# Optimization experiments

Measured on AMD Instinct MI355X. Metric: run time of the kernel, lower is better.

Reference implementation:

```python
import jax, jax.numpy as jnp
import numpy as np

_DN = ('NCHW', 'OIHW', 'NCHW')

def _conv(x, w, b, stride, pad):
    y = jax.lax.conv_general_dilated(x, w, (stride, stride), [(pad, pad), (pad, pad)], dimension_numbers=_DN)
    return y + b[None, :, None, None]

def setup_inputs() -> dict:
    key = jax.random.key(0)
    ks = jax.random.split(key, 9)
    B, C, H, W = 32, 3, 128, 128
    HC, D, K = 128, 64, 512
    def he(k, shape, fan_in):
        return jax.random.normal(k, shape, jnp.float32) * np.float32(np.sqrt(2.0 / fan_in))
    return {
        'x': jax.random.normal(ks[0], (B, C, H, W), jnp.float32),
        'enc_w1': he(ks[1], (HC, C, 3, 3), C * 9),
        'enc_b1': jnp.zeros((HC,), jnp.float32),
        'enc_w2': he(ks[2], (HC, HC, 3, 3), HC * 9),
        'enc_b2': jnp.zeros((HC,), jnp.float32),
        'proj_w': he(ks[3], (D, HC, 1, 1), HC),
        'proj_b': jnp.zeros((D,), jnp.float32),
        'codebook': jax.random.uniform(ks[4], (K, D), jnp.float32, -1.0 / K, 1.0 / K),
        'dproj_w': he(ks[5], (HC, D, 1, 1), D),
        'dproj_b': jnp.zeros((HC,), jnp.float32),
        'dconv1_w': he(ks[6], (HC, HC, 3, 3), HC * 9),
        'dconv1_b': jnp.zeros((HC,), jnp.float32),
        'dconv2_w': he(ks[7], (C, HC, 1, 1), HC),
        'dconv2_b': jnp.zeros((C,), jnp.float32),
    }

def reference(x, enc_w1, enc_b1, enc_w2, enc_b2, proj_w, proj_b, codebook,
              dproj_w, dproj_b, dconv1_w, dconv1_b, dconv2_w, dconv2_b):
    beta = 0.25
    Gh = Gw = 8
    B, C, H, W = x.shape
    D = codebook.shape[1]
    sg = jax.lax.stop_gradient
    # ---- encoder ----
    h = jax.nn.relu(_conv(x, enc_w1, enc_b1, 2, 1))      # (B,HC,H/2,W/2)
    h = jax.nn.relu(_conv(h, enc_w2, enc_b2, 2, 1))      # (B,HC,H/4,W/4)
    f = h.shape[2] // Gh                                  # adaptive avg pool (exact)
    h = h.reshape(B, h.shape[1], Gh, f, Gw, f).mean(axis=(3, 5))
    z_e = _conv(h, proj_w, proj_b, 1, 0)                 # (B,D,Gh,Gw)
    # ---- vector quantizer ----
    z_flat = z_e.transpose(0, 2, 3, 1).reshape(-1, D)    # (B*Gh*Gw, D)
    dist = ((z_flat ** 2).sum(1, keepdims=True)
            + (codebook ** 2).sum(1)[None, :]
            - 2.0 * (z_flat @ codebook.T))               # (N, K)
    idx_flat = jnp.argmin(dist, axis=1)
    z_q_flat = codebook[idx_flat]                        # gather
    codebook_loss = jnp.mean((z_q_flat - sg(z_flat)) ** 2)
    commit_loss = jnp.mean((z_flat - sg(z_q_flat)) ** 2)
    vq_loss = codebook_loss + beta * commit_loss
    z_q_st = z_flat + sg(z_q_flat - z_flat)              # straight-through
    z_q = z_q_st.reshape(B, Gh, Gw, D).transpose(0, 3, 1, 2)
    idx = idx_flat.reshape(B, Gh, Gw)
    # ---- decoder ----
    y = _conv(z_q, dproj_w, dproj_b, 1, 0)               # (B,HC,Gh,Gw)
    s = H // Gh                                           # nearest upsample factor
    y = jnp.repeat(jnp.repeat(y, s, axis=2), s, axis=3)  # (B,HC,H,W)
    y = jax.nn.relu(y)
    y = jax.nn.relu(_conv(y, dconv1_w, dconv1_b, 1, 1))
    x_hat = _conv(y, dconv2_w, dconv2_b, 1, 0)           # (B,C,H,W)
    return (x_hat, idx, vq_loss, z_e)
```

## Files before the change

### kernel.cpp

```cpp
#include <hip/hip_runtime.h>
#include <math.h>


typedef _Float16 f16x8 __attribute__((ext_vector_type(8)));
typedef float f32x4 __attribute__((ext_vector_type(4)));

#define H1N 16777216
#define YTAIL (2048 * 128)

__global__ __launch_bounds__(256) void k_prep(const float* __restrict__ w2,
                                              const float* __restrict__ w1,
                                              const float* __restrict__ wp,
                                              const float* __restrict__ wd,
                                              const float* __restrict__ wd1,
                                              const float* __restrict__ cb,
                                              float* __restrict__ w1t,
                                              float* __restrict__ wpT,
                                              float* __restrict__ wdT,
                                              float* __restrict__ cbT,
                                              _Float16* __restrict__ Ah,
                                              _Float16* __restrict__ WS,
                                              _Float16* __restrict__ h1h) {
  int bx = blockIdx.x, tid = threadIdx.x;
  if (bx < 128) {
    __shared__ float wrow[1152];
    int co = bx;
    for (int i = tid; i < 1152; i += 256) wrow[i] = wd1[co * 1152 + i];
    __syncthreads();
    if (tid < 128) {
      int ci = tid;
      float w[9];
#pragma unroll
      for (int t = 0; t < 9; t++) w[t] = wrow[ci * 9 + t];
      float rx[3][5];
#pragma unroll
      for (int ky = 0; ky < 3; ky++) {
        float a0 = w[ky * 3 + 0], a1 = w[ky * 3 + 1], a2 = w[ky * 3 + 2];
        rx[ky][0] = a0; rx[ky][1] = a1 + a2; rx[ky][2] = a0 + a1 + a2;
        rx[ky][3] = a0 + a1; rx[ky][4] = a2;
      }
#pragma unroll
      for (int px = 0; px < 5; px++) {
        float s0 = rx[0][px], s1 = rx[1][px], s2 = rx[2][px];
        float ry[5];
        ry[0] = s0; ry[1] = s1 + s2; ry[2] = s0 + s1 + s2; ry[3] = s0 + s1; ry[4] = s2;
#pragma unroll
        for (int py = 0; py < 5; py++) {
          int pq = py * 5 + px;
          int o = (pq * 128 + co) * 128 + ci;
          Ah[o] = (_Float16)ry[py];
        }
      }
    }
    return;
  }
  if (bx < 144) {
    __shared__ float wst[9216];
    int co0 = (bx - 128) * 8;
    for (int i = tid; i < 9216; i += 256) wst[i] = w2[co0 * 1152 + i];
    __syncthreads();
    for (int i = tid; i < 9216; i += 256) {
      int co = i / 1152, r = i - co * 1152;
      int tap = r >> 7, ci = r & 127;
      float v = wst[co * 1152 + ci * 9 + tap];
      int og = ((tap * 16 + (ci >> 3)) * 128 + co0 + co) * 8 + (ci & 7);
      WS[og] = (_Float16)v;
    }
    return;
  }
  if (bx < 152) {
    __shared__ float cbs[64 * 65];
    int k0 = (bx - 144) * 64;
    for (int i = tid; i < 4096; i += 256) {
      int k = i >> 6, d = i & 63;
      cbs[k * 65 + d] = cb[(k0 + k) * 64 + d];
    }
    __syncthreads();
    for (int i = tid; i < 4096; i += 256) {
      int d = i >> 6, k = i & 63;
      cbT[d * 512 + k0 + k] = cbs[k * 65 + d];
    }
    return;
  }
  for (int i = tid; i < 3456; i += 256) {
    int co = i & 127, t = i >> 7;
    w1t[t * 128 + co] = w1[co * 27 + t];
  }
  for (int i = tid; i < 8192; i += 256) {
    int d = i & 63, k = i >> 6;
    wpT[k * 64 + d] = wp[d * 128 + k];
  }
  for (int i = tid; i < 8192; i += 256) {
    int co = i & 127, d = i >> 7;
    wdT[d * 128 + co] = wd[co * 64 + d];
  }
  if (tid < 64) h1h[H1N + tid] = (_Float16)0.f;
}

__global__ __launch_bounds__(256) void k_conv1(const float* __restrict__ x,
                                               const float* __restrict__ w1t,
                                               const float* __restrict__ b1,
                                               _Float16* __restrict__ h1h) {
  __shared__ float E[3][9][68];
  __shared__ float O[3][9][68];
  int co_t = blockIdx.x, oh_t = blockIdx.y, b = blockIdx.z;
  int oh0 = oh_t * 4;
  int tid = threadIdx.x;
  int wv = __builtin_amdgcn_readfirstlane(tid >> 6);
  int l = tid & 63;
  int coB = co_t * 32 + wv * 8;

  for (int idx = tid; idx < 1728; idx += 256) {
    int p = idx & 63, r = idx >> 6;
    int ci = r / 9, lr = r - ci * 9;
    int ih = 2 * oh0 - 1 + lr;
    float2 v = make_float2(0.f, 0.f);
    if ((unsigned)ih < 128u)
      v = *(const float2*)&x[((b * 3 + ci) * 128 + ih) * 128 + 2 * p];
    E[ci][lr][p] = v.x;
    O[ci][lr][p + 1] = v.y;
  }
  if (tid < 27) {
    int ci = tid / 9, lr = tid - ci * 9;
    O[ci][lr][0] = 0.f;
  }
  __syncthreads();

  int ohl = l >> 4, ow0 = (l & 15) * 4;
  int oh = oh0 + ohl;
  float4 acc[8];
#pragma unroll
  for (int q = 0; q < 8; q++) {
    float bv = b1[coB + q];
    acc[q] = make_float4(bv, bv, bv, bv);
  }
#pragma unroll
  for (int ci = 0; ci < 3; ci++) {
#pragma unroll
    for (int ky = 0; ky < 3; ky++) {
      int lr = 2 * ohl + ky;
      float4 ev = *(float4*)&E[ci][lr][ow0];
      float4 od = *(float4*)&O[ci][lr][ow0];
      float o4 = O[ci][lr][ow0 + 4];
      const float* wr = w1t + (ci * 9 + ky * 3) * 128 + coB;
#pragma unroll
      for (int q = 0; q < 8; q++) {
        float wa = wr[q], wb = wr[128 + q], wc = wr[256 + q];
        acc[q].x = fmaf(wa, od.x, acc[q].x);
        acc[q].x = fmaf(wb, ev.x, acc[q].x);
        acc[q].x = fmaf(wc, od.y, acc[q].x);
        acc[q].y = fmaf(wa, od.y, acc[q].y);
        acc[q].y = fmaf(wb, ev.y, acc[q].y);
        acc[q].y = fmaf(wc, od.z, acc[q].y);
        acc[q].z = fmaf(wa, od.z, acc[q].z);
        acc[q].z = fmaf(wb, ev.z, acc[q].z);
        acc[q].z = fmaf(wc, od.w, acc[q].z);
        acc[q].w = fmaf(wa, od.w, acc[q].w);
        acc[q].w = fmaf(wb, ev.w, acc[q].w);
        acc[q].w = fmaf(wc, o4,   acc[q].w);
      }
    }
  }
  int g = coB >> 3;
  int pbase = ((g * 32 + b) * 64 + oh) * 64;
#pragma unroll
  for (int oi = 0; oi < 4; oi++) {
    f16x8 hv;
#pragma unroll
    for (int q = 0; q < 8; q++)
      hv[q] = (_Float16)fmaxf(((const float*)&acc[q])[oi], 0.f);
    *(f16x8*)&h1h[(pbase + ow0 + oi) * 8] = hv;
  }
}

#define C2_ACHUNK 4420
#define C2_WCHUNK 2340
#define C2_WOFF (C2_ACHUNK * 8)
#define C2_LDSB ((C2_ACHUNK + C2_WCHUNK) * 16)
#define C2_STEP 4194304
#define C2_WADV 4096

__global__ __launch_bounds__(512, 2) void k_conv2(const _Float16* __restrict__ h1h,
                                                  const _Float16* __restrict__ WS,
                                                  const float* __restrict__ b2,
                                                  float* __restrict__ h2p) {
  extern __shared__ _Float16 L[];
  int bx = blockIdx.x;
  int cohalf = bx & 1;
  int bq = bx >> 1;
  int b = bq >> 2, ohq = bq & 3;
  int oh0 = ohq * 8;
  int tid = threadIdx.x;
  int w = tid >> 6, l = tid & 63;
  int cw = w & 1, rw = w >> 1;
  int ln = l & 15, quad = l >> 4;

  int cursA[9];
  int advA[9];
#pragma unroll
  for (int k = 0; k < 9; k++) {
    int c = (k < 8) ? (tid + k * 512) : (4096 + tid);
    if (c < C2_ACHUNK) {
      int q = c / 65, rem = c - q * 65;
      int ph = rem >= 33;
      int u = ph ? rem - 33 : rem;
      int r = q % 17, g = q / 17;
      int iw = ph ? 2 * u : 2 * u - 1;
      int ih = 2 * oh0 - 1 + r;
      bool ok = (ih >= 0) && (iw >= 0) && (iw < 64);
      cursA[k] = ok ? ((g * 32 + b) * 64 + ih) * 512 + iw * 8 : H1N;
      advA[k] = ok ? C2_STEP : 0;
    } else {
      cursA[k] = H1N;
      advA[k] = 0;
    }
  }
  int cursW[5];
#pragma unroll
  for (int k = 0; k < 5; k++) {
    int c = (k < 4) ? (tid + k * 512) : (2048 + tid);
    if (c < C2_WCHUNK) {
      int q65 = c / 65, u = c - q65 * 65;
      if (u > 63) u = 63;
      int t = q65 >> 2, ci8 = q65 & 3;
      cursW[k] = (t * 16 + ci8) * 1024 + (cohalf * 64 + u) * 8;
    } else {
      cursW[k] = 0;
    }
  }

  f32x4 acc[2][4] = {};
  for (int step = 0; step < 4; step++) {
    if (step) __syncthreads();
#pragma unroll
    for (int k = 0; k < 8; k++) {
      __builtin_amdgcn_global_load_lds(
          (const __attribute__((address_space(1))) void*)(h1h + cursA[k]),
          (__attribute__((address_space(3))) void*)&L[(tid + k * 512) * 8],
          16, 0, 0);
      cursA[k] += advA[k];
    }
    if (tid < 324)
      __builtin_amdgcn_global_load_lds(
          (const __attribute__((address_space(1))) void*)(h1h + cursA[8]),
          (__attribute__((address_space(3))) void*)&L[(4096 + tid) * 8],
          16, 0, 0);
    cursA[8] += advA[8];
#pragma unroll
    for (int k = 0; k < 4; k++) {
      __builtin_amdgcn_global_load_lds(
          (const __attribute__((address_space(1))) void*)(WS + cursW[k]),
          (__attribute__((address_space(3))) void*)&L[C2_WOFF +
                                                     (tid + k * 512) * 8],
          16, 0, 0);
      cursW[k] += C2_WADV;
    }
    if (tid < 292)
      __builtin_amdgcn_global_load_lds(
          (const __attribute__((address_space(1))) void*)(WS + cursW[4]),
          (__attribute__((address_space(3))) void*)&L[C2_WOFF +
                                                     (2048 + tid) * 8],
          16, 0, 0);
    cursW[4] += C2_WADV;
    __syncthreads();

#pragma unroll
    for (int ky = 0; ky < 3; ky++) {
#pragma unroll
      for (int kx = 0; kx < 3; kx++) {
        int t = ky * 3 + kx;
        int wb = (t * 4 + quad) * 65 + cw * 32 + ln;
        f16x8 Ah0 = *(const f16x8*)&L[C2_WOFF + wb * 8];
        f16x8 Ah1 = *(const f16x8*)&L[C2_WOFF + (wb + 16) * 8];
#pragma unroll
        for (int s = 0; s < 4; s++) {
          int owl = (s & 1) * 16 + ln;
          int r = 4 * rw + 2 * (s >> 1) + ky;
          int abase = (quad * 17 + r) * 65;
          int uoff = (kx == 1) ? (33 + owl) : (owl + (kx == 2));
          f16x8 Bh = *(const f16x8*)&L[(abase + uoff) * 8];
          acc[0][s] = __builtin_amdgcn_mfma_f32_16x16x32_f16(Ah0, Bh, acc[0][s], 0, 0, 0);
          acc[1][s] = __builtin_amdgcn_mfma_f32_16x16x32_f16(Ah1, Bh, acc[1][s], 0, 0, 0);
        }
      }
    }
  }
  __syncthreads();
  float* h2s = (float*)L;
#pragma unroll
  for (int cs = 0; cs < 2; cs++)
#pragma unroll
    for (int s = 0; s < 4; s++) {
      int row = 2 * rw + (s >> 1);
      int col = (s & 1) * 16 + ln;
#pragma unroll
      for (int r2 = 0; r2 < 4; r2++) {
        int co64 = cw * 32 + cs * 16 + quad * 4 + r2;
        int co = cohalf * 64 + co64;
        h2s[(co64 * 8 + row) * 32 + col] = fmaxf(acc[cs][s][r2] + b2[co], 0.f);
      }
    }
  __syncthreads();
  for (int c = tid; c < 1024; c += 512) {
    int co64 = c >> 4, rem = c & 15;
    int pr = rem >> 3, pc = rem & 7;
    const float* base = &h2s[(co64 * 8 + pr * 4) * 32 + pc * 4];
    float s = 0.f;
#pragma unroll
    for (int rr = 0; rr < 4; rr++) {
      s += base[rr * 32 + 0];
      s += base[rr * 32 + 1];
      s += base[rr * 32 + 2];
      s += base[rr * 32 + 3];
    }
    h2p[((b * 128 + cohalf * 64 + co64) * 8 + (2 * ohq + pr)) * 8 + pc] =
        s * 0.0625f;
  }
}

__global__ __launch_bounds__(256) void k_poolproj(const float* __restrict__ h2p,
                                                  const float* __restrict__ wpT,
                                                  const float* __restrict__ pb,
                                                  float* __restrict__ z_e_out,
                                                  float* __restrict__ lossacc) {
  __shared__ float hp[128][16];
  __shared__ float Ws[128][64];
  int bx = blockIdx.x, tid = threadIdx.x;
  int b = bx >> 2, quarter = bx & 3;
  if (bx == 0 && tid == 0) lossacc[0] = 0.f;
  for (int i = tid; i < 8192; i += 256) Ws[i >> 6][i & 63] = wpT[i];
  for (int i = tid; i < 2048; i += 256) {
    int ci = i >> 4, pl = i & 15;
    hp[ci][pl] = h2p[(b * 128 + ci) * 64 + quarter * 16 + pl];
  }
  __syncthreads();
  int d = tid >> 2, s0 = (tid & 3) * 4;
  float4 acc = make_float4(0.f, 0.f, 0.f, 0.f);
  for (int k = 0; k < 128; k++) {
    float a = Ws[k][d];
    float4 h = *(float4*)&hp[k][s0];
    acc.x = fmaf(a, h.x, acc.x);
    acc.y = fmaf(a, h.y, acc.y);
    acc.z = fmaf(a, h.z, acc.z);
    acc.w = fmaf(a, h.w, acc.w);
  }
  float bv = pb[d];
  float4 r4 = make_float4(acc.x + bv, acc.y + bv, acc.z + bv, acc.w + bv);
  *(float4*)&z_e_out[(b * 64 + d) * 64 + quarter * 16 + s0] = r4;
}

__global__ __launch_bounds__(256) void k_vqdproj(const float* __restrict__ z_e,
                                                 const float* __restrict__ cbT,
                                                 const float* __restrict__ cb,
                                                 const float* __restrict__ wdT,
                                                 const float* __restrict__ db,
                                                 float* __restrict__ idx_f,
                                                 _Float16* __restrict__ Yh,
                                                 float* __restrict__ loss_acc) {
  __shared__ float zs[64];
  __shared__ float zqv[64];
  __shared__ double wbst[4];
  __shared__ int wbi[4];
  int n = blockIdx.x, tid = threadIdx.x;
  int b = n >> 6, pi = n & 63;
  if (tid < 64) zs[tid] = z_e[(b * 64 + tid) * 64 + pi];
  if (n == 0 && tid < 64) {
    Yh[YTAIL + tid] = (_Float16)0.f;
    Yh[YTAIL + 64 + tid] = (_Float16)0.f;
  }
  __syncthreads();
  int w = tid >> 6, lane = tid & 63;
  double best = 1e300;
  int bi = 0;
#pragma unroll
  for (int j = 0; j < 2; j++) {
    int k = w * 128 + j * 64 + lane;
    double a0 = 0.0, a1 = 0.0, a2 = 0.0, a3 = 0.0;
#pragma unroll 4
    for (int d = 0; d < 64; d += 4) {
      double f0 = (double)zs[d] - (double)cbT[d * 512 + k];
      double f1 = (double)zs[d + 1] - (double)cbT[(d + 1) * 512 + k];
      double f2 = (double)zs[d + 2] - (double)cbT[(d + 2) * 512 + k];
      double f3 = (double)zs[d + 3] - (double)cbT[(d + 3) * 512 + k];
      a0 = fma(f0, f0, a0);
      a1 = fma(f1, f1, a1);
      a2 = fma(f2, f2, a2);
      a3 = fma(f3, f3, a3);
    }
    double acc = (a0 + a1) + (a2 + a3);
    if (acc < best) { best = acc; bi = k; }
  }
  for (int m = 1; m < 64; m <<= 1) {
    double ob = __shfl_xor(best, m, 64);
    int oi = __shfl_xor(bi, m, 64);
    if (ob < best || (ob == best && oi < bi)) { best = ob; bi = oi; }
  }
  if (lane == 0) { wbst[w] = best; wbi[w] = bi; }
  __syncthreads();
  best = wbst[0];
  bi = wbi[0];
#pragma unroll
  for (int q = 1; q < 4; q++) {
    double ob = wbst[q];
    int oi = wbi[q];
    if (ob < best || (ob == best && oi < bi)) { best = ob; bi = oi; }
  }
  if (tid < 64) {
    float zq_l = cb[bi * 64 + tid];
    float e = zq_l - zs[tid];
    float sq = e * e;
    for (int m = 1; m < 64; m <<= 1) sq += __shfl_xor(sq, m, 64);
    if (tid == 0) {
      idx_f[n] = (float)bi;
      atomicAdd(loss_acc, sq);
    }
    zqv[tid] = zq_l;
  }
  __syncthreads();
  if (tid < 128) {
    float a = db[tid];
#pragma unroll 4
    for (int d = 0; d < 64; d++) a = fmaf(wdT[d * 128 + tid], zqv[d], a);
    Yh[n * 128 + tid] = (_Float16)fmaxf(a, 0.f);
  }
}

__global__ __launch_bounds__(256) void k_dec(const _Float16* __restrict__ Yh,
                                             const _Float16* __restrict__ Ah,
                                             const float* __restrict__ bc1,
                                             float* __restrict__ Tb) {
  int bxx = blockIdx.x;
  int cls = bxx >> 6, n_t = bxx & 63;
  int rc = cls / 3, c3 = cls - rc * 3;
  const int rset[3][2] = {{0, 1}, {2, 2}, {3, 4}};
  const int rcnt[3] = {2, 1, 2};
  int w = threadIdx.x >> 6, l = threadIdx.x & 63;
  int ln = l & 15, quad = l >> 4;
  int coW = w * 32;
  int nB = n_t * 32;
  int kq = quad * 8;
  f32x4 acc[2][2] = {};
  for (int iy = 0; iy < rcnt[rc]; iy++) {
    int py = rset[rc][iy];
    int dy = (py == 0) ? -1 : ((py == 4) ? 1 : 0);
    for (int ix = 0; ix < rcnt[c3]; ix++) {
      int px = rset[c3][ix];
      int dx = (px == 0) ? -1 : ((px == 4) ? 1 : 0);
      int pq = py * 5 + px;
      int src[2];
#pragma unroll
      for (int s = 0; s < 2; s++) {
        int n = nB + s * 16 + ln;
        int bb = n >> 6, s6 = n & 63;
        int sy = (s6 >> 3) + dy, sx = (s6 & 7) + dx;
        bool ok = ((unsigned)sy < 8u) && ((unsigned)sx < 8u);
        src[s] = ok ? ((bb * 64 + sy * 8 + sx) * 128) : YTAIL;
      }
#pragma unroll 2
      for (int ci0 = 0; ci0 < 128; ci0 += 32) {
        const int wbase = (pq * 128 + coW + ln) * 128 + ci0 + kq;
        f16x8 Ah0 = *(const f16x8*)&Ah[wbase];
        f16x8 Ah1 = *(const f16x8*)&Ah[wbase + 2048];
        f16x8 Bh[2];
#pragma unroll
        for (int s = 0; s < 2; s++)
          Bh[s] = *(const f16x8*)&Yh[src[s] + ci0 + kq];
#pragma unroll
        for (int cs = 0; cs < 2; cs++) {
          f16x8 ah = cs ? Ah1 : Ah0;
#pragma unroll
          for (int s = 0; s < 2; s++)
            acc[cs][s] = __builtin_amdgcn_mfma_f32_16x16x32_f16(ah, Bh[s], acc[cs][s], 0, 0, 0);
        }
      }
    }
  }
#pragma unroll
  for (int cs = 0; cs < 2; cs++)
#pragma unroll
    for (int s = 0; s < 2; s++) {
      int site = nB + s * 16 + ln;
      int co0 = coW + cs * 16 + quad * 4;
      float4 bv = *(const float4*)&bc1[co0];
      float4 g = make_float4(fmaxf(acc[cs][s][0] + bv.x, 0.f),
                             fmaxf(acc[cs][s][1] + bv.y, 0.f),
                             fmaxf(acc[cs][s][2] + bv.z, 0.f),
                             fmaxf(acc[cs][s][3] + bv.w, 0.f));
      *(float4*)&Tb[(cls * 2048 + site) * 128 + co0] = g;
    }
}

__global__ __launch_bounds__(256) void k_out(const float* __restrict__ TbG,
                                             const float* __restrict__ w3,
                                             const float* __restrict__ b3,
                                             float* __restrict__ xhat,
                                             const float* __restrict__ loss_acc,
                                             float* __restrict__ out_loss) {
  __shared__ float Tb[9][128];
  __shared__ float part[9][3][8];
  __shared__ float vals[9][3];
  int bj = blockIdx.x, bi = blockIdx.y, b = blockIdx.z;
  int s = bi * 8 + bj;
  int n = b * 64 + s;
  int tid = threadIdx.x;
  if (bj == 0 && bi == 0 && b == 0 && tid == 0)
    out_loss[0] = loss_acc[0] * 1.25f / 131072.0f;
  for (int i = tid; i < 1152; i += 256) {
    int cls = i >> 7, co = i & 127;
    Tb[cls][co] = TbG[(cls * 2048 + n) * 128 + co];
  }
  __syncthreads();
  if (tid < 216) {
    int cls = tid / 24, rem = tid - cls * 24;
    int cc = rem >> 3, seg = rem & 7;
    float ss = 0.f;
#pragma unroll
    for (int d = 0; d < 16; d++) ss = fmaf(w3[cc * 128 + seg * 16 + d], Tb[cls][seg * 16 + d], ss);
    part[cls][cc][seg] = ss;
  }
  __syncthreads();
  if (tid < 27) {
    int cls = tid / 3, cc = tid - cls * 3;
    float ss = b3[cc];
#pragma unroll
    for (int seg = 0; seg < 8; seg++) ss += part[cls][cc][seg];
    vals[cls][cc] = ss;
  }
  __syncthreads();
  for (int i = tid; i < 768; i += 256) {
    int cc = i >> 8, p = i & 255;
    int ry = p >> 4, rx = p & 15;
    int rcls = (ry == 0) ? 0 : ((ry == 15) ? 2 : 1);
    int ccls = (rx == 0) ? 0 : ((rx == 15) ? 2 : 1);
    xhat[((b * 3 + cc) * 128 + bi * 16 + ry) * 128 + bj * 16 + rx] =
        vals[rcls * 3 + ccls][cc];
  }
}

extern "C" void kernel_launch(void* const* d_in, const int* in_sizes, int n_in,
                              void* d_out, int out_size, void* d_ws, size_t ws_size,
                              hipStream_t stream) {
  const float* x   = (const float*)d_in[0];
  const float* w1  = (const float*)d_in[1];
  const float* b1  = (const float*)d_in[2];
  const float* w2  = (const float*)d_in[3];
  const float* b2  = (const float*)d_in[4];
  const float* wp  = (const float*)d_in[5];
  const float* pb  = (const float*)d_in[6];
  const float* cb  = (const float*)d_in[7];
  const float* wd  = (const float*)d_in[8];
  const float* db  = (const float*)d_in[9];
  const float* wc1 = (const float*)d_in[10];
  const float* bc1 = (const float*)d_in[11];
  const float* wc2 = (const float*)d_in[12];
  const float* bc2 = (const float*)d_in[13];
  float* out = (float*)d_out;
  float* ws  = (float*)d_ws;

  _Float16* h1h = (_Float16*)(ws);
  float* h2p    = ws + 16777280;
  _Float16* WS  = (_Float16*)(ws + 20971584);
  float* w1t    = ws + 21119040;
  float* wpT    = ws + 21122496;
  float* wdT    = ws + 21130688;
  float* cbT    = ws + 21138880;
  _Float16* Ahd = (_Float16*)(ws + 21171648);
  float* Tb      = ws;
  _Float16* Yh   = (_Float16*)(ws + 6553600);
  float* lossacc = ws + 6815872;

  float* o_xhat = out;
  float* o_idx  = out + 1572864;
  float* o_loss = out + 1574912;
  float* o_ze   = out + 1574913;

  static bool s_attr_done = false;
  if (!s_attr_done) {
    (void)hipFuncSetAttribute((const void*)k_conv2,
                              hipFuncAttributeMaxDynamicSharedMemorySize, C2_LDSB);
    s_attr_done = true;
  }

  k_prep<<<dim3(153), 256, 0, stream>>>(w2, w1, wp, wd, wc1, cb,
                                        w1t, wpT, wdT, cbT, Ahd, WS, h1h);
  k_conv1<<<dim3(4, 16, 32), 256, 0, stream>>>(x, w1t, b1, h1h);
  k_conv2<<<dim3(256), 512, C2_LDSB, stream>>>(h1h, WS, b2, h2p);
  k_poolproj<<<dim3(128), 256, 0, stream>>>(h2p, wpT, pb, o_ze, lossacc);
  k_vqdproj<<<dim3(2048), 256, 0, stream>>>(o_ze, cbT, cb, wdT, db, o_idx, Yh, lossacc);
  k_dec<<<dim3(576), 256, 0, stream>>>(Yh, Ahd, bc1, Tb);
  k_out<<<dim3(8, 8, 32), 256, 0, stream>>>(Tb, wc2, bc2, o_xhat, lossacc, o_loss);
}
```

Before: 201.9 us.

## Rewrite first encoder conv as fp16 MFMA implicit GEMM

The first conv (3->128 channels, stride 2) moves from scalar fp32 FMAs to an im2col-in-LDS implicit GEMM using 16x16x32 f16 MFMA, with K=27 padded to 32. The weights are pre-packed as fp16 in the prep kernel, and each block now handles one output row for all 128 output channels. Outputs go through an LDS tile so the grouped fp16 layout is written with wide stores. This lowers the input and weights to fp16 precision before the multiply, which adds rounding error against the fp32 reference.

```diff
diff --git a/kernel.cpp b/kernel.cpp
--- a/kernel.cpp
+++ b/kernel.cpp
@@ -2,6 +2,7 @@
 #include <math.h>
 
 
+typedef _Float16 f16x4 __attribute__((ext_vector_type(4)));
 typedef _Float16 f16x8 __attribute__((ext_vector_type(8)));
 typedef float f32x4 __attribute__((ext_vector_type(4)));
 
@@ -14,7 +15,7 @@
                                               const float* __restrict__ wd,
                                               const float* __restrict__ wd1,
                                               const float* __restrict__ cb,
-                                              float* __restrict__ w1t,
+                                              _Float16* __restrict__ w1A,
                                               float* __restrict__ wpT,
                                               float* __restrict__ wdT,
                                               float* __restrict__ cbT,
@@ -82,9 +83,9 @@
     }
     return;
   }
-  for (int i = tid; i < 3456; i += 256) {
-    int co = i & 127, t = i >> 7;
-    w1t[t * 128 + co] = w1[co * 27 + t];
+  for (int i = tid; i < 4096; i += 256) {
+    int co = i >> 5, k = i & 31;
+    w1A[i] = (k < 27) ? (_Float16)w1[co * 27 + k] : (_Float16)0.f;
   }
   for (int i = tid; i < 8192; i += 256) {
     int d = i & 63, k = i >> 6;
@@ -98,78 +99,77 @@
 }
 
 __global__ __launch_bounds__(256) void k_conv1(const float* __restrict__ x,
-                                               const float* __restrict__ w1t,
+                                               const _Float16* __restrict__ w1A,
                                                const float* __restrict__ b1,
                                                _Float16* __restrict__ h1h) {
-  __shared__ float E[3][9][68];
-  __shared__ float O[3][9][68];
-  int co_t = blockIdx.x, oh_t = blockIdx.y, b = blockIdx.z;
-  int oh0 = oh_t * 4;
+  __shared__ _Float16 xs[3][3][132];
+  __shared__ _Float16 J[64 * 40];
+  __shared__ _Float16 As[128 * 40];
+  __shared__ _Float16 Cs[64 * 136];
+  int oh = blockIdx.x, b = blockIdx.y;
   int tid = threadIdx.x;
-  int wv = __builtin_amdgcn_readfirstlane(tid >> 6);
-  int l = tid & 63;
-  int coB = co_t * 32 + wv * 8;
-
-  for (int idx = tid; idx < 1728; idx += 256) {
-    int p = idx & 63, r = idx >> 6;
-    int ci = r / 9, lr = r - ci * 9;
-    int ih = 2 * oh0 - 1 + lr;
-    float2 v = make_float2(0.f, 0.f);
-    if ((unsigned)ih < 128u)
-      v = *(const float2*)&x[((b * 3 + ci) * 128 + ih) * 128 + 2 * p];
-    E[ci][lr][p] = v.x;
-    O[ci][lr][p + 1] = v.y;
-  }
-  if (tid < 27) {
-    int ci = tid / 9, lr = tid - ci * 9;
-    O[ci][lr][0] = 0.f;
-  }
-  __syncthreads();
-
-  int ohl = l >> 4, ow0 = (l & 15) * 4;
-  int oh = oh0 + ohl;
-  float4 acc[8];
-#pragma unroll
-  for (int q = 0; q < 8; q++) {
-    float bv = b1[coB + q];
-    acc[q] = make_float4(bv, bv, bv, bv);
-  }
-#pragma unroll
-  for (int ci = 0; ci < 3; ci++) {
-#pragma unroll
-    for (int ky = 0; ky < 3; ky++) {
-      int lr = 2 * ohl + ky;
-      float4 ev = *(float4*)&E[ci][lr][ow0];
-      float4 od = *(float4*)&O[ci][lr][ow0];
-      float o4 = O[ci][lr][ow0 + 4];
-      const float* wr = w1t + (ci * 9 + ky * 3) * 128 + coB;
-#pragma unroll
-      for (int q = 0; q < 8; q++) {
-        float wa = wr[q], wb = wr[128 + q], wc = wr[256 + q];
-        acc[q].x = fmaf(wa, od.x, acc[q].x);
-        acc[q].x = fmaf(wb, ev.x, acc[q].x);
-        acc[q].x = fmaf(wc, od.y, acc[q].x);
-        acc[q].y = fmaf(wa, od.y, acc[q].y);
-        acc[q].y = fmaf(wb, ev.y, acc[q].y);
-        acc[q].y = fmaf(wc, od.z, acc[q].y);
-        acc[q].z = fmaf(wa, od.z, acc[q].z);
-        acc[q].z = fmaf(wb, ev.z, acc[q].z);
-        acc[q].z = fmaf(wc, od.w, acc[q].z);
-        acc[q].w = fmaf(wa, od.w, acc[q].w);
-        acc[q].w = fmaf(wb, ev.w, acc[q].w);
-        acc[q].w = fmaf(wc, o4,   acc[q].w);
-      }
-    }
-  }
-  int g = coB >> 3;
-  int pbase = ((g * 32 + b) * 64 + oh) * 64;
-#pragma unroll
-  for (int oi = 0; oi < 4; oi++) {
-    f16x8 hv;
-#pragma unroll
-    for (int q = 0; q < 8; q++)
-      hv[q] = (_Float16)fmaxf(((const float*)&acc[q])[oi], 0.f);
-    *(f16x8*)&h1h[(pbase + ow0 + oi) * 8] = hv;
+  int w = tid >> 6, l = tid & 63;
+  int ln = l & 15, quad = l >> 4;
+  int coW = w * 32;
+  int kq = quad * 8;
+
+  for (int i = tid; i < 1152; i += 256) {
+    int ci = i / 384, rem = i - ci * 384;
+    int r = rem >> 7, iw = rem & 127;
+    int ih = 2 * oh - 1 + r;
+    float v = ((unsigned)ih < 128u) ? x[((b * 3 + ci) * 128 + ih) * 128 + iw] : 0.f;
+    xs[ci][r][1 + iw] = (_Float16)v;
+  }
+  if (tid < 9) {
+    int ci = tid / 3, r = tid - ci * 3;
+    xs[ci][r][0] = (_Float16)0.f;
+  }
+  for (int i = tid; i < 4096; i += 256) {
+    int co = i >> 5, k = i & 31;
+    As[co * 40 + k] = w1A[i];
+  }
+  __syncthreads();
+  for (int i = tid; i < 2048; i += 256) {
+    int px = i >> 5, k = i & 31;
+    _Float16 v = (_Float16)0.f;
+    if (k < 27) {
+      int ci = k / 9, t = k - ci * 9;
+      int ky = t / 3, kx = t - ky * 3;
+      v = xs[ci][ky][2 * px + kx];
+    }
+    J[px * 40 + k] = v;
+  }
+  __syncthreads();
+  f32x4 acc[2][4] = {};
+#pragma unroll
+  for (int cs = 0; cs < 2; cs++) {
+    f16x8 a = *(const f16x8*)&As[(coW + cs * 16 + ln) * 40 + kq];
+#pragma unroll
+    for (int pt = 0; pt < 4; pt++) {
+      f16x8 bfr = *(const f16x8*)&J[(pt * 16 + ln) * 40 + kq];
+      acc[cs][pt] = __builtin_amdgcn_mfma_f32_16x16x32_f16(a, bfr, acc[cs][pt], 0, 0, 0);
+    }
+  }
+#pragma unroll
+  for (int cs = 0; cs < 2; cs++) {
+    int co0 = coW + cs * 16 + quad * 4;
+    float4 bv = *(const float4*)&b1[co0];
+#pragma unroll
+    for (int pt = 0; pt < 4; pt++) {
+      int px = pt * 16 + ln;
+      f16x4 v;
+      v[0] = (_Float16)fmaxf(acc[cs][pt][0] + bv.x, 0.f);
+      v[1] = (_Float16)fmaxf(acc[cs][pt][1] + bv.y, 0.f);
+      v[2] = (_Float16)fmaxf(acc[cs][pt][2] + bv.z, 0.f);
+      v[3] = (_Float16)fmaxf(acc[cs][pt][3] + bv.w, 0.f);
+      *(f16x4*)&Cs[px * 136 + co0] = v;
+    }
+  }
+  __syncthreads();
+  for (int i = tid; i < 1024; i += 256) {
+    int g = i >> 6, px = i & 63;
+    f16x8 v = *(const f16x8*)&Cs[px * 136 + g * 8];
+    *(f16x8*)&h1h[(((g * 32 + b) * 64 + oh) * 64 + px) * 8] = v;
   }
 }
 
@@ -560,7 +560,7 @@
   _Float16* h1h = (_Float16*)(ws);
   float* h2p    = ws + 16777280;
   _Float16* WS  = (_Float16*)(ws + 20971584);
-  float* w1t    = ws + 21119040;
+  _Float16* w1A = (_Float16*)(ws + 21119040);
   float* wpT    = ws + 21122496;
   float* wdT    = ws + 21130688;
   float* cbT    = ws + 21138880;
@@ -582,8 +582,8 @@
   }
 
   k_prep<<<dim3(153), 256, 0, stream>>>(w2, w1, wp, wd, wc1, cb,
-                                        w1t, wpT, wdT, cbT, Ahd, WS, h1h);
-  k_conv1<<<dim3(4, 16, 32), 256, 0, stream>>>(x, w1t, b1, h1h);
+                                        w1A, wpT, wdT, cbT, Ahd, WS, h1h);
+  k_conv1<<<dim3(64, 32), 256, 0, stream>>>(x, w1A, b1, h1h);
   k_conv2<<<dim3(256), 512, C2_LDSB, stream>>>(h1h, WS, b2, h2p);
   k_poolproj<<<dim3(128), 256, 0, stream>>>(h2p, wpT, pb, o_ze, lossacc);
   k_vqdproj<<<dim3(2048), 256, 0, stream>>>(o_ze, cbT, cb, wdT, db, o_idx, Yh, lossacc);
```

Result: no change. 199.5 us (-1.2%).
